# Kernel optimization log

Measured on AMD Instinct MI355X. Metric: run time of the kernel, lower is better.

Reference implementation:

```python
import jax, jax.numpy as jnp
import numpy as np

B, S, HID = 1, 2048, 2048
H, KVH, D = 16, 8, 128
N_REP = H // KVH
SCALING = float(np.sqrt(D))  # head_dim ** 0.5 (nGPT uses positive exponent)
SQK_INIT_VALUE = 1.0
SQK_INIT_SCALING = 0.02
EPS = 1e-8


def _rotate_half(x):
    x1, x2 = jnp.split(x, 2, axis=-1)
    return jnp.concatenate((-x2, x1), axis=-1)


def setup_inputs() -> dict:
    key = jax.random.key(0)
    ks = jax.random.split(key, 8)
    hidden_states = jax.random.normal(ks[0], (B, S, HID), dtype=jnp.float32)
    # realistic RoPE tables, full rotary (rotary_dim == head_dim)
    inv_freq = 1.0 / (10000.0 ** (np.arange(0, D, 2, dtype=np.float32) / D))
    t = np.arange(S, dtype=np.float32)
    freqs = np.outer(t, inv_freq)                      # [S, D/2]
    emb = np.concatenate([freqs, freqs], axis=-1)      # [S, D]
    cos = jnp.asarray(np.cos(emb))[None].repeat(B, 0)  # [B, S, D]
    sin = jnp.asarray(np.sin(emb))[None].repeat(B, 0)
    # additive causal mask [B, 1, S, S]
    causal = jnp.tril(jnp.ones((S, S), dtype=bool))
    attention_mask = jnp.where(causal, 0.0, jnp.finfo(jnp.float32).min)[None, None].repeat(B, 0)
    sd = 0.02
    Wq = jax.random.normal(ks[1], (H * D, HID), dtype=jnp.float32) * sd
    Wk = jax.random.normal(ks[2], (KVH * D, HID), dtype=jnp.float32) * sd
    Wv = jax.random.normal(ks[3], (KVH * D, HID), dtype=jnp.float32) * sd
    Wo = jax.random.normal(ks[4], (HID, H * D), dtype=jnp.float32) * sd
    sqk_w = jnp.full((H * D,), SQK_INIT_SCALING, dtype=jnp.float32)  # Linear(1, H*D) weight, init constant
    return {"hidden_states": hidden_states, "cos": cos, "sin": sin,
            "attention_mask": attention_mask, "Wq": Wq, "Wk": Wk, "Wv": Wv,
            "Wo": Wo, "sqk_w": sqk_w}


def _l2_normalize(x):
    return x / (jnp.linalg.norm(x, axis=-1, keepdims=True) + EPS)


def reference(hidden_states, cos, sin, attention_mask, Wq, Wk, Wv, Wo, sqk_w):
    b, s, _ = hidden_states.shape
    # projections (torch Linear: y = x @ W.T)
    q = jnp.einsum('bsd,ed->bse', hidden_states, Wq).reshape(b, s, H, D).transpose(0, 2, 1, 3)
    k = jnp.einsum('bsd,ed->bse', hidden_states, Wk).reshape(b, s, KVH, D).transpose(0, 2, 1, 3)
    v = jnp.einsum('bsd,ed->bse', hidden_states, Wv).reshape(b, s, KVH, D).transpose(0, 2, 1, 3)
    # RoPE, cos/sin broadcast over heads: [B,1,S,D]
    c, sn = cos[:, None], sin[:, None]
    q = q * c + _rotate_half(q) * sn
    k = k * c + _rotate_half(k) * sn
    # nGPT: L2-normalize q,k; learnable per-channel scale on q
    sqk = (sqk_w * (SQK_INIT_VALUE / SQK_INIT_SCALING)).reshape(1, H, 1, D)
    q = _l2_normalize(q) * sqk ** 2
    k = _l2_normalize(k)
    # GQA: repeat kv heads
    k = jnp.repeat(k, N_REP, axis=1)
    v = jnp.repeat(v, N_REP, axis=1)
    scores = jnp.einsum('bhqd,bhkd->bhqk', q, k) * SCALING
    scores = scores + attention_mask
    attn = jax.nn.softmax(scores.astype(jnp.float32), axis=-1).astype(q.dtype)
    out = jnp.einsum('bhqk,bhkd->bhqd', attn, v)
    out = out.transpose(0, 2, 1, 3).reshape(b, s, H * D)
    return jnp.einsum('bse,de->bsd', out, Wo)
```

## Files before the change

### kernel.cpp

```cpp
#include <hip/hip_runtime.h>

typedef unsigned short u16;
typedef __attribute__((ext_vector_type(4))) float f32x4;
typedef __attribute__((ext_vector_type(8))) __bf16 bf16x8;
typedef __attribute__((ext_vector_type(8))) u16 u16x8;
typedef __attribute__((ext_vector_type(4))) u16 u16x4;

#define S_LEN 2048
#define NH 16
#define NKV 8
#define QSCALE_LOG2E 16.322118857f
#define M2INIT 16.6f
#define EXP2(x) __builtin_amdgcn_exp2f(x)

#define AS1(p) ((const __attribute__((address_space(1))) void*)(p))
#define AS3(p) ((__attribute__((address_space(3))) void*)(p))

__device__ __forceinline__ float b2f(u16 u) {
    return __uint_as_float(((unsigned int)u) << 16);
}
__device__ __forceinline__ u16 f2b(float f) {
    unsigned int x = __float_as_uint(f);
    unsigned int r = (x + 0x7FFFu + ((x >> 16) & 1u)) >> 16;
    return (u16)r;
}

__global__ __launch_bounds__(256) void cast_all(const float* __restrict__ hs,
                                                const float* __restrict__ Wq,
                                                const float* __restrict__ Wk,
                                                const float* __restrict__ Wv,
                                                const float* __restrict__ Wo,
                                                u16* __restrict__ hsb,
                                                u16* __restrict__ wcat,
                                                u16* __restrict__ wob) {
    int i = blockIdx.x * 256 + threadIdx.x;
    const float* src; u16* dst; int off;
    if (i < 1048576)      { src = hs; dst = hsb;            off = i; }
    else if (i < 2097152) { src = Wq; dst = wcat;           off = i - 1048576; }
    else if (i < 2621440) { src = Wk; dst = wcat + 4194304; off = i - 2097152; }
    else if (i < 3145728) { src = Wv; dst = wcat + 6291456; off = i - 2621440; }
    else                  { src = Wo; dst = wob;            off = i - 3145728; }
    f32x4 v = reinterpret_cast<const f32x4*>(src)[off];
    u16x4 o;
    o[0] = f2b(v[0]); o[1] = f2b(v[1]); o[2] = f2b(v[2]); o[3] = f2b(v[3]);
    reinterpret_cast<u16x4*>(dst)[off] = o;
}

__global__ __launch_bounds__(256) void cast_v_t(const float* __restrict__ qkvf,
                                                u16* __restrict__ vt) {
    __shared__ float tile[64][65];
    int s0 = (blockIdx.x & 31) * 64;
    int c0 = (blockIdx.x >> 5) * 64;
    for (int i = threadIdx.x; i < 64 * 64; i += 256) {
        int r = i >> 6, c = i & 63;
        tile[r][c] = qkvf[(size_t)(s0 + r) * 4096 + 3072 + c0 + c];
    }
    __syncthreads();
    for (int i = threadIdx.x; i < 64 * 64; i += 256) {
        int r = i >> 6, c = i & 63;
        vt[(size_t)(c0 + r) * 2048 + s0 + c] = f2b(tile[c][r]);
    }
}

template<int BM, int BN, int WM, int WN>
__global__ __launch_bounds__(256) void gemm_t(const u16* __restrict__ A,
                                              const u16* __restrict__ B,
                                              float* __restrict__ C,
                                              int M, int N, int K) {
    constexpr int MR = BM / WM / 16;
    constexpr int NR = BN / WN / 16;
    __shared__ alignas(16) u16 As[2][BM * 64];
    __shared__ alignas(16) u16 Bs[2][BN * 64];
    int tid = threadIdx.x, lane = tid & 63, wave = tid >> 6;
    int row0 = blockIdx.y * BM, col0 = blockIdx.x * BN;
    int wr = (wave / WN) * (BM / WM);
    int wc = (wave % WN) * (BN / WN);
    int l15 = lane & 15, lg = lane >> 4;

    f32x4 acc[MR][NR] = {};

    auto stage = [&](int bf, int k0) {
#pragma unroll
        for (int i = 0; i < BM / 32; i++) {
            int slot = i * 4 + wave;
            int r = slot * 8 + (lane >> 3);
            int c = lane & 7;
            __builtin_amdgcn_global_load_lds(AS1(A + (size_t)(row0 + r) * K + k0 + c * 8),
                                             AS3(&As[bf][slot * 512]), 16, 0, 0);
        }
#pragma unroll
        for (int i = 0; i < BN / 32; i++) {
            int slot = i * 4 + wave;
            int r = slot * 8 + (lane >> 3);
            int c = lane & 7;
            __builtin_amdgcn_global_load_lds(AS1(B + (size_t)(col0 + r) * K + k0 + c * 8),
                                             AS3(&Bs[bf][slot * 512]), 16, 0, 0);
        }
    };

    stage(0, 0);
    __syncthreads();

    int nk = K >> 6, buf = 0;
    for (int t = 0; t < nk; ++t) {
        if (t + 1 < nk) stage(buf ^ 1, (t + 1) * 64);

        __builtin_amdgcn_s_setprio(1);
#pragma unroll
        for (int kk = 0; kk < 2; kk++) {
            bf16x8 af[MR], bg[NR];
#pragma unroll
            for (int m = 0; m < MR; m++)
                af[m] = *reinterpret_cast<const bf16x8*>(&As[buf][(wr + m * 16 + l15) * 64 + kk * 32 + lg * 8]);
#pragma unroll
            for (int n = 0; n < NR; n++)
                bg[n] = *reinterpret_cast<const bf16x8*>(&Bs[buf][(wc + n * 16 + l15) * 64 + kk * 32 + lg * 8]);
#pragma unroll
            for (int m = 0; m < MR; m++)
#pragma unroll
                for (int n = 0; n < NR; n++)
                    acc[m][n] = __builtin_amdgcn_mfma_f32_16x16x32_bf16(af[m], bg[n], acc[m][n], 0, 0, 0);
        }
        __builtin_amdgcn_s_setprio(0);

        __syncthreads();
        buf ^= 1;
    }

#pragma unroll
    for (int m = 0; m < MR; m++)
#pragma unroll
        for (int n = 0; n < NR; n++)
#pragma unroll
            for (int r = 0; r < 4; r++) {
                int row = row0 + wr + m * 16 + lg * 4 + r;
                int col = col0 + wc + n * 16 + l15;
                C[(size_t)row * N + col] = acc[m][n][r];
            }
}

__global__ __launch_bounds__(256) void rope_norm(const float* __restrict__ qkvf,
                                                 const float* __restrict__ cosb,
                                                 const float* __restrict__ sinb,
                                                 const float* __restrict__ sqkw,
                                                 u16* __restrict__ qb,
                                                 u16* __restrict__ kb) {
    int w = blockIdx.x * 4 + (threadIdx.x >> 6);
    int lane = threadIdx.x & 63;
    bool isQ = w < 32768;
    const float* src;
    int s, hg;
    if (isQ) { hg = w & (NH - 1); s = w >> 4; src = qkvf + (size_t)s * 4096 + hg * 128; }
    else     { int w2 = w - 32768; hg = w2 & (NKV - 1); s = w2 >> 3; src = qkvf + (size_t)s * 4096 + 2048 + hg * 128; }
    float x0 = src[lane], x1 = src[lane + 64];
    float c0 = cosb[s * 128 + lane], c1 = cosb[s * 128 + 64 + lane];
    float s0 = sinb[s * 128 + lane], s1 = sinb[s * 128 + 64 + lane];
    float y0 = x0 * c0 - x1 * s0;
    float y1 = x1 * c1 + x0 * s1;
    float ss = y0 * y0 + y1 * y1;
#pragma unroll
    for (int off = 32; off; off >>= 1) ss += __shfl_xor(ss, off);
    float inv = 1.f / (sqrtf(ss) + 1e-8f);
    if (isQ) {
        float w0 = sqkw[hg * 128 + lane] * 50.f;
        float w1 = sqkw[hg * 128 + 64 + lane] * 50.f;
        u16* dst = qb + ((size_t)hg * S_LEN + s) * 128;
        dst[lane]      = f2b(y0 * inv * w0 * w0 * QSCALE_LOG2E);
        dst[lane + 64] = f2b(y1 * inv * w1 * w1 * QSCALE_LOG2E);
    } else {
        u16* dst = kb + ((size_t)hg * S_LEN + s) * 128;
        dst[lane]      = f2b(y0 * inv);
        dst[lane + 64] = f2b(y1 * inv);
    }
}

__global__ __launch_bounds__(256) void attn_mfma(const u16* __restrict__ Qb,
                                                 const u16* __restrict__ Kb,
                                                 const u16* __restrict__ Vt,
                                                 u16* __restrict__ Ao) {
    __shared__ alignas(16) u16 Ks[64 * 128];
    __shared__ alignas(16) u16 Vs[128 * 64];
    __shared__ alignas(16) u16 Pb[4][16][72];

    int tid = threadIdx.x, lane = tid & 63, wv = tid >> 6;
    int h = blockIdx.x & (NH - 1);
    int z = blockIdx.x >> 4;
    int qi = (z < 16) ? (31 - z) : (z - 16);
    int qb0 = qi * 64;
    int g = h >> 1;
    int l15 = lane & 15, lg = lane >> 4;

    bf16x8 qf[4];
    {
        const u16* qrow = Qb + ((size_t)h * S_LEN + qb0 + wv * 16 + l15) * 128;
#pragma unroll
        for (int kd = 0; kd < 4; kd++)
            qf[kd] = *reinterpret_cast<const bf16x8*>(qrow + kd * 32 + lg * 8);
    }

    const u16* kbase = Kb + (size_t)g * S_LEN * 128;
    const u16* vbase = Vt + (size_t)g * 128 * S_LEN;

    int rk = wv * 16 + (lane >> 4);
    int ck = lane & 15;
    int rv = wv * 32 + (lane >> 3);
    int cv = lane & 7;

    u16x8 kreg[4], vreg[4];

    float m2[4], lpart[4];
    f32x4 oacc[8];
#pragma unroll
    for (int r = 0; r < 4; r++) { m2[r] = M2INIT; lpart[r] = 0.f; }
#pragma unroll
    for (int dt = 0; dt < 8; dt++) oacc[dt] = (f32x4){0.f, 0.f, 0.f, 0.f};

    int nt = qi + 1;

#pragma unroll
    for (int i = 0; i < 4; i++) {
        kreg[i] = *reinterpret_cast<const u16x8*>(kbase + (size_t)(rk + 4 * i) * 128 + ck * 8);
        vreg[i] = *reinterpret_cast<const u16x8*>(vbase + (size_t)(rv + 8 * i) * S_LEN + cv * 8);
    }

    for (int t = 0; t < nt; ++t) {
        int k0 = t * 64;
        __syncthreads();
#pragma unroll
        for (int i = 0; i < 4; i++) {
            int r = rk + 4 * i;
            *reinterpret_cast<u16x8*>((char*)Ks + r * 256 + ((ck * 16) ^ ((r & 7) << 4))) = kreg[i];
            int r2 = rv + 8 * i;
            *reinterpret_cast<u16x8*>((char*)Vs + r2 * 128 + ((cv * 16) ^ ((r2 & 7) << 4))) = vreg[i];
        }
        __syncthreads();

        if (t + 1 < nt) {
            int kn = k0 + 64;
#pragma unroll
            for (int i = 0; i < 4; i++) {
                kreg[i] = *reinterpret_cast<const u16x8*>(kbase + (size_t)(kn + rk + 4 * i) * 128 + ck * 8);
                vreg[i] = *reinterpret_cast<const u16x8*>(vbase + (size_t)(rv + 8 * i) * S_LEN + kn + cv * 8);
            }
        }

        f32x4 sacc[4];
#pragma unroll
        for (int kt = 0; kt < 4; kt++) sacc[kt] = (f32x4){0.f, 0.f, 0.f, 0.f};
        __builtin_amdgcn_s_setprio(1);
#pragma unroll
        for (int kt = 0; kt < 4; kt++) {
            int r = kt * 16 + l15;
#pragma unroll
            for (int kd = 0; kd < 4; kd++) {
                int col = kd * 64 + lg * 16;
                bf16x8 kf = *reinterpret_cast<const bf16x8*>((char*)Ks + r * 256 + (col ^ ((r & 7) << 4)));
                sacc[kt] = __builtin_amdgcn_mfma_f32_16x16x32_bf16(qf[kd], kf, sacc[kt], 0, 0, 0);
            }
        }
        __builtin_amdgcn_s_setprio(0);

        if (t == nt - 1) {
#pragma unroll
            for (int kt = 0; kt < 4; kt++)
#pragma unroll
                for (int r = 0; r < 4; r++) {
                    int key = k0 + kt * 16 + l15;
                    int q = qb0 + wv * 16 + lg * 4 + r;
                    if (key > q) sacc[kt][r] = -1e30f;
                }
        }

        int need = 0;
#pragma unroll
        for (int r = 0; r < 4; r++) {
            float tm = fmaxf(fmaxf(sacc[0][r], sacc[1][r]), fmaxf(sacc[2][r], sacc[3][r]));
            need |= (tm > m2[r] + 11.5f) ? 1 : 0;
        }
        if (__builtin_expect(__any(need), 0)) {
#pragma unroll
            for (int r = 0; r < 4; r++) {
                float tm = fmaxf(fmaxf(sacc[0][r], sacc[1][r]), fmaxf(sacc[2][r], sacc[3][r]));
                tm = fmaxf(tm, __shfl_xor(tm, 1));
                tm = fmaxf(tm, __shfl_xor(tm, 2));
                tm = fmaxf(tm, __shfl_xor(tm, 4));
                tm = fmaxf(tm, __shfl_xor(tm, 8));
                float mn = fmaxf(m2[r], tm);
                float sc = EXP2(m2[r] - mn);
                m2[r] = mn;
                lpart[r] *= sc;
#pragma unroll
                for (int dt = 0; dt < 8; dt++) oacc[dt][r] *= sc;
            }
        }
        float pnew[4][4];
#pragma unroll
        for (int r = 0; r < 4; r++) {
            float p0 = EXP2(sacc[0][r] - m2[r]);
            float p1 = EXP2(sacc[1][r] - m2[r]);
            float p2 = EXP2(sacc[2][r] - m2[r]);
            float p3 = EXP2(sacc[3][r] - m2[r]);
            pnew[0][r] = p0; pnew[1][r] = p1; pnew[2][r] = p2; pnew[3][r] = p3;
            lpart[r] += (p0 + p1) + (p2 + p3);
        }

#pragma unroll
        for (int kt = 0; kt < 4; kt++)
#pragma unroll
            for (int r = 0; r < 4; r++)
                Pb[wv][lg * 4 + r][kt * 16 + l15] = f2b(pnew[kt][r]);

        __builtin_amdgcn_s_setprio(1);
#pragma unroll
        for (int ks = 0; ks < 2; ks++) {
            bf16x8 pf = *reinterpret_cast<const bf16x8*>(&Pb[wv][l15][ks * 32 + lg * 8]);
#pragma unroll
            for (int dt = 0; dt < 8; dt++) {
                int r = dt * 16 + l15;
                int col = ks * 64 + lg * 16;
                bf16x8 vf = *reinterpret_cast<const bf16x8*>((char*)Vs + r * 128 + (col ^ ((r & 7) << 4)));
                oacc[dt] = __builtin_amdgcn_mfma_f32_16x16x32_bf16(pf, vf, oacc[dt], 0, 0, 0);
            }
        }
        __builtin_amdgcn_s_setprio(0);
    }

    float inv[4];
#pragma unroll
    for (int r = 0; r < 4; r++) {
        float ls = lpart[r];
        ls += __shfl_xor(ls, 1);
        ls += __shfl_xor(ls, 2);
        ls += __shfl_xor(ls, 4);
        ls += __shfl_xor(ls, 8);
        inv[r] = 1.f / ls;
    }
#pragma unroll
    for (int dt = 0; dt < 8; dt++)
#pragma unroll
        for (int r = 0; r < 4; r++) {
            int q = qb0 + wv * 16 + lg * 4 + r;
            Ao[(size_t)q * 2048 + h * 128 + dt * 16 + l15] = f2b(oacc[dt][r] * inv[r]);
        }
}

extern "C" void kernel_launch(void* const* d_in, const int* in_sizes, int n_in,
                              void* d_out, int out_size, void* d_ws, size_t ws_size,
                              hipStream_t stream) {
    const float* hs   = (const float*)d_in[0];
    const float* cosb = (const float*)d_in[1];
    const float* sinb = (const float*)d_in[2];
    const float* Wq   = (const float*)d_in[4];
    const float* Wk   = (const float*)d_in[5];
    const float* Wv   = (const float*)d_in[6];
    const float* Wo   = (const float*)d_in[7];
    const float* sqkw = (const float*)d_in[8];

    char* ws = (char*)d_ws;
    u16*   hsb  = (u16*)(ws);
    u16*   wcat = (u16*)(ws + 8388608);
    u16*   wob  = (u16*)(ws + 25165824);
    float* qkvf = (float*)(ws + 33554432);
    u16*   qb   = (u16*)(ws + 67108864);
    u16*   kb   = (u16*)(ws + 75497472);
    u16*   vt   = (u16*)(ws + 79691776);
    u16*   ao   = (u16*)(ws + 83886080);

    cast_all<<<16384, 256, 0, stream>>>(hs, Wq, Wk, Wv, Wo, hsb, wcat, wob);

    gemm_t<128, 128, 2, 2><<<dim3(32, 16), 256, 0, stream>>>(hsb, wcat, qkvf, 2048, 4096, 2048);

    rope_norm<<<12288, 256, 0, stream>>>(qkvf, cosb, sinb, sqkw, qb, kb);
    cast_v_t<<<512, 256, 0, stream>>>(qkvf, vt);

    attn_mfma<<<512, 256, 0, stream>>>(qb, kb, vt, ao);

    gemm_t<128, 64, 4, 1><<<dim3(32, 16), 256, 0, stream>>>(ao, wob, (float*)d_out, 2048, 2048, 2048);
}
```

Baseline: 174.1 us.

## Fuse RoPE, L2 norm, and V transpose into the QKV projection GEMM epilogue

Replaces the fp32 QKV GEMM output plus separate rope_norm and cast_v_t kernels with a single GEMM whose epilogue applies RoPE, L2 normalization, q scaling and bf16 conversion directly from accumulators. Each block owns a full 128-wide head, with waves tiled 4x1, so the rotate-half pairing and the norm reduction stay within the wave's registers. V tiles are written transposed as bf16. This removes a 32 MB fp32 intermediate round trip and two launches, at the cost of a different warp layout (4x1 instead of 2x2) and scattered 2-byte epilogue stores.

```diff
diff --git a/kernel.cpp b/kernel.cpp
--- a/kernel.cpp
+++ b/kernel.cpp
@@ -46,19 +46,128 @@
     reinterpret_cast<u16x4*>(dst)[off] = o;
 }
 
-__global__ __launch_bounds__(256) void cast_v_t(const float* __restrict__ qkvf,
+__global__ __launch_bounds__(256) void gemm_qkv(const u16* __restrict__ A,
+                                                const u16* __restrict__ B,
+                                                const float* __restrict__ cosb,
+                                                const float* __restrict__ sinb,
+                                                const float* __restrict__ sqkw,
+                                                u16* __restrict__ qb,
+                                                u16* __restrict__ kb,
                                                 u16* __restrict__ vt) {
-    __shared__ float tile[64][65];
-    int s0 = (blockIdx.x & 31) * 64;
-    int c0 = (blockIdx.x >> 5) * 64;
-    for (int i = threadIdx.x; i < 64 * 64; i += 256) {
-        int r = i >> 6, c = i & 63;
-        tile[r][c] = qkvf[(size_t)(s0 + r) * 4096 + 3072 + c0 + c];
-    }
+    const int K = 2048;
+    __shared__ alignas(16) u16 As[2][128 * 64];
+    __shared__ alignas(16) u16 Bs[2][128 * 64];
+    int tid = threadIdx.x, lane = tid & 63, wave = tid >> 6;
+    int row0 = blockIdx.y * 128, col0 = blockIdx.x * 128;
+    int wr = wave * 32;
+    int l15 = lane & 15, lg = lane >> 4;
+
+    f32x4 acc[2][8] = {};
+
+    auto stage = [&](int bf, int k0) {
+#pragma unroll
+        for (int i = 0; i < 4; i++) {
+            int slot = i * 4 + wave;
+            int r = slot * 8 + (lane >> 3);
+            int c = lane & 7;
+            __builtin_amdgcn_global_load_lds(AS1(A + (size_t)(row0 + r) * K + k0 + c * 8),
+                                             AS3(&As[bf][slot * 512]), 16, 0, 0);
+            __builtin_amdgcn_global_load_lds(AS1(B + (size_t)(col0 + r) * K + k0 + c * 8),
+                                             AS3(&Bs[bf][slot * 512]), 16, 0, 0);
+        }
+    };
+
+    stage(0, 0);
     __syncthreads();
-    for (int i = threadIdx.x; i < 64 * 64; i += 256) {
-        int r = i >> 6, c = i & 63;
-        vt[(size_t)(c0 + r) * 2048 + s0 + c] = f2b(tile[c][r]);
+
+    int nk = K >> 6, buf = 0;
+    for (int t = 0; t < nk; ++t) {
+        if (t + 1 < nk) stage(buf ^ 1, (t + 1) * 64);
+
+        __builtin_amdgcn_s_setprio(1);
+#pragma unroll
+        for (int kk = 0; kk < 2; kk++) {
+            bf16x8 af[2], bg[8];
+#pragma unroll
+            for (int m = 0; m < 2; m++)
+                af[m] = *reinterpret_cast<const bf16x8*>(&As[buf][(wr + m * 16 + l15) * 64 + kk * 32 + lg * 8]);
+#pragma unroll
+            for (int n = 0; n < 8; n++)
+                bg[n] = *reinterpret_cast<const bf16x8*>(&Bs[buf][(n * 16 + l15) * 64 + kk * 32 + lg * 8]);
+#pragma unroll
+            for (int m = 0; m < 2; m++)
+#pragma unroll
+                for (int n = 0; n < 8; n++)
+                    acc[m][n] = __builtin_amdgcn_mfma_f32_16x16x32_bf16(af[m], bg[n], acc[m][n], 0, 0, 0);
+        }
+        __builtin_amdgcn_s_setprio(0);
+
+        __syncthreads();
+        buf ^= 1;
+    }
+
+    int bx = blockIdx.x;
+    if (bx < 24) {
+        bool isQ = bx < 16;
+        float w2[8];
+        if (isQ) {
+#pragma unroll
+            for (int j = 0; j < 8; j++) {
+                float w = sqkw[bx * 128 + j * 16 + l15] * 50.f;
+                w2[j] = w * w * QSCALE_LOG2E;
+            }
+        }
+        u16* outb = isQ ? (qb + (size_t)bx * S_LEN * 128)
+                        : (kb + (size_t)(bx - 16) * S_LEN * 128);
+#pragma unroll
+        for (int m = 0; m < 2; m++)
+#pragma unroll
+            for (int r = 0; r < 4; r++) {
+                int s = row0 + wr + m * 16 + lg * 4 + r;
+                const float* crow = cosb + (size_t)s * 128;
+                const float* srow = sinb + (size_t)s * 128;
+                float y[8];
+                float ss = 0.f;
+#pragma unroll
+                for (int j = 0; j < 4; j++) {
+                    float c  = crow[j * 16 + l15];
+                    float sn = srow[j * 16 + l15];
+                    float x0 = acc[m][j][r], x1 = acc[m][j + 4][r];
+                    float a = x0 * c - x1 * sn;
+                    float b = x1 * c + x0 * sn;
+                    y[j] = a; y[j + 4] = b;
+                    ss += a * a + b * b;
+                }
+                ss += __shfl_xor(ss, 1);
+                ss += __shfl_xor(ss, 2);
+                ss += __shfl_xor(ss, 4);
+                ss += __shfl_xor(ss, 8);
+                float inv = 1.f / (sqrtf(ss) + 1e-8f);
+                u16* orow = outb + (size_t)s * 128;
+                if (isQ) {
+#pragma unroll
+                    for (int j = 0; j < 8; j++)
+                        orow[j * 16 + l15] = f2b(y[j] * inv * w2[j]);
+                } else {
+#pragma unroll
+                    for (int j = 0; j < 8; j++)
+                        orow[j * 16 + l15] = f2b(y[j] * inv);
+                }
+            }
+    } else {
+        int g = bx - 24;
+#pragma unroll
+        for (int n = 0; n < 8; n++) {
+            int d = n * 16 + l15;
+            u16* vrow = vt + (size_t)(g * 128 + d) * S_LEN;
+#pragma unroll
+            for (int m = 0; m < 2; m++) {
+                u16x4 pk;
+#pragma unroll
+                for (int r = 0; r < 4; r++) pk[r] = f2b(acc[m][n][r]);
+                *reinterpret_cast<u16x4*>(&vrow[row0 + wr + m * 16 + lg * 4]) = pk;
+            }
+        }
     }
 }
 
@@ -139,41 +248,6 @@
             }
 }
 
-__global__ __launch_bounds__(256) void rope_norm(const float* __restrict__ qkvf,
-                                                 const float* __restrict__ cosb,
-                                                 const float* __restrict__ sinb,
-                                                 const float* __restrict__ sqkw,
-                                                 u16* __restrict__ qb,
-                                                 u16* __restrict__ kb) {
-    int w = blockIdx.x * 4 + (threadIdx.x >> 6);
-    int lane = threadIdx.x & 63;
-    bool isQ = w < 32768;
-    const float* src;
-    int s, hg;
-    if (isQ) { hg = w & (NH - 1); s = w >> 4; src = qkvf + (size_t)s * 4096 + hg * 128; }
-    else     { int w2 = w - 32768; hg = w2 & (NKV - 1); s = w2 >> 3; src = qkvf + (size_t)s * 4096 + 2048 + hg * 128; }
-    float x0 = src[lane], x1 = src[lane + 64];
-    float c0 = cosb[s * 128 + lane], c1 = cosb[s * 128 + 64 + lane];
-    float s0 = sinb[s * 128 + lane], s1 = sinb[s * 128 + 64 + lane];
-    float y0 = x0 * c0 - x1 * s0;
-    float y1 = x1 * c1 + x0 * s1;
-    float ss = y0 * y0 + y1 * y1;
-#pragma unroll
-    for (int off = 32; off; off >>= 1) ss += __shfl_xor(ss, off);
-    float inv = 1.f / (sqrtf(ss) + 1e-8f);
-    if (isQ) {
-        float w0 = sqkw[hg * 128 + lane] * 50.f;
-        float w1 = sqkw[hg * 128 + 64 + lane] * 50.f;
-        u16* dst = qb + ((size_t)hg * S_LEN + s) * 128;
-        dst[lane]      = f2b(y0 * inv * w0 * w0 * QSCALE_LOG2E);
-        dst[lane + 64] = f2b(y1 * inv * w1 * w1 * QSCALE_LOG2E);
-    } else {
-        u16* dst = kb + ((size_t)hg * S_LEN + s) * 128;
-        dst[lane]      = f2b(y0 * inv);
-        dst[lane + 64] = f2b(y1 * inv);
-    }
-}
-
 __global__ __launch_bounds__(256) void attn_mfma(const u16* __restrict__ Qb,
                                                  const u16* __restrict__ Kb,
                                                  const u16* __restrict__ Vt,
@@ -360,18 +434,14 @@
     u16*   hsb  = (u16*)(ws);
     u16*   wcat = (u16*)(ws + 8388608);
     u16*   wob  = (u16*)(ws + 25165824);
-    float* qkvf = (float*)(ws + 33554432);
-    u16*   qb   = (u16*)(ws + 67108864);
-    u16*   kb   = (u16*)(ws + 75497472);
-    u16*   vt   = (u16*)(ws + 79691776);
-    u16*   ao   = (u16*)(ws + 83886080);
+    u16*   qb   = (u16*)(ws + 33554432);
+    u16*   kb   = (u16*)(ws + 41943040);
+    u16*   vt   = (u16*)(ws + 46137344);
+    u16*   ao   = (u16*)(ws + 50331648);
 
     cast_all<<<16384, 256, 0, stream>>>(hs, Wq, Wk, Wv, Wo, hsb, wcat, wob);
 
-    gemm_t<128, 128, 2, 2><<<dim3(32, 16), 256, 0, stream>>>(hsb, wcat, qkvf, 2048, 4096, 2048);
-
-    rope_norm<<<12288, 256, 0, stream>>>(qkvf, cosb, sinb, sqkw, qb, kb);
-    cast_v_t<<<512, 256, 0, stream>>>(qkvf, vt);
+    gemm_qkv<<<dim3(32, 16), 256, 0, stream>>>(hsb, wcat, cosb, sinb, sqkw, qb, kb, vt);
 
     attn_mfma<<<512, 256, 0, stream>>>(qb, kb, vt, ao);
 
```

After: 163.9 us. 5.9% less time.
